# Optimization experiments

Measured on AMD Instinct MI355X. Metric: run time of the kernel, lower is better.

The kernel has to match this reference:

```python
import jax, jax.numpy as jnp
import numpy as np

ALPHA, BETA, LAMB, GAMMA = 1.0, 1.0, 1e-4, 1.0
K_NN, TAU = 50, 0.1
EPS = 1e-8


def _sqdist(A, B):
    # ||a - b||^2, clamped at 0 like the torch code
    d2 = (A * A).sum(1)[:, None] + (B * B).sum(1)[None, :] - 2.0 * (A @ B.T)
    return jnp.maximum(d2, 0.0)


def _mmd(s, t):
    comb = jnp.concatenate([s, t], axis=0)
    sigma_sq = jax.lax.stop_gradient(jnp.median(_sqdist(comb, comb))) / 2.0
    sigma_sq = jnp.where(sigma_sq < 1e-6, jnp.float32(1.0), sigma_sq)
    g = 1.0 / (sigma_sq + EPS)
    kxx = jnp.exp(-g * _sqdist(s, s)).mean()
    kyy = jnp.exp(-g * _sqdist(t, t)).mean()
    kxy = jnp.exp(-g * _sqdist(s, t)).mean()
    return jnp.maximum(kxx + kyy - 2.0 * kxy, 0.0)


def setup_inputs() -> dict:
    key = jax.random.key(0)
    ks = jax.random.split(key, 8)
    B, d, N, Nq, K = 256, 128, 200000, 10000, K_NN
    q_batch = jax.random.normal(ks[0], (B, d), jnp.float32)
    X = jax.random.normal(ks[1], (N, d), jnp.float32)
    W = jax.random.normal(ks[2], (d, d), jnp.float32) * (1.0 / np.sqrt(d))
    b = jnp.zeros((d,), jnp.float32)
    pre_weights = jax.random.uniform(ks[3], (Nq, K), jnp.float32)
    pre_weights = pre_weights / pre_weights.sum(1, keepdims=True)
    pre_indices = jax.random.randint(ks[4], (Nq, K), 0, N)
    q_indices = jax.random.randint(ks[5], (B,), 0, Nq)
    idx = jax.random.randint(ks[6], (B,), 0, N)
    return {"q_batch": q_batch, "X": X, "W": W, "b": b,
            "pre_weights": pre_weights, "pre_indices": pre_indices,
            "q_indices": q_indices, "idx": idx}


def reference(q_batch, X, W, b, pre_weights, pre_indices, q_indices, idx):
    Tq = q_batch @ W.T + b                                   # model(q_batch), Linear(d, d)
    # ---- MMD between mapped queries and a random database batch ----
    loss_dist = _mmd(Tq, X[idx])
    # ---- exact KNN (faiss IndexFlatL2 equivalent) on detached embeddings ----
    d2_all = _sqdist(jax.lax.stop_gradient(Tq), X)           # [B, N]
    _, post_idx = jax.lax.top_k(-d2_all, K_NN)               # [B, K] nearest neighbors
    Xn = X[post_idx]                                         # [B, K, d]
    l2 = ((Tq[:, None, :] - Xn) ** 2).sum(-1)                # [B, K] (grad flows here)
    post_w = jax.nn.softmax(-l2 / TAU, axis=1)
    # ---- union-KL, vectorized over batch (exact torch.unique semantics) ----
    pre_i = pre_indices[q_indices]                           # [B, K]
    pre_w = pre_weights[q_indices]                           # [B, K]
    cat = jnp.concatenate([pre_i, post_idx], axis=1)         # [B, 2K]
    # multiplicity of each id within the concatenated list -> collapse duplicates
    mult = (cat[:, :, None] == cat[:, None, :]).sum(-1).astype(jnp.float32)  # [B, 2K]
    p_raw = jnp.einsum('bmk,bk->bm',
                       (cat[:, :, None] == pre_i[:, None, :]).astype(jnp.float32), pre_w)
    q_raw = jnp.einsum('bmk,bk->bm',
                       (cat[:, :, None] == post_idx[:, None, :]).astype(jnp.float32), post_w)
    p_c = jnp.maximum(p_raw, EPS)
    q_c = jnp.maximum(q_raw, EPS)
    p = p_c / (p_c / mult).sum(1, keepdims=True)             # normalize over union
    q = q_c / (q_c / mult).sum(1, keepdims=True)
    kl = ((p * (jnp.log(p) - jnp.log(q))) / mult).sum(1)     # KL(p || q) per sample
    loss_knn = kl.mean()
    # ---- L2 regularization of model params & anchor loss ----
    loss_reg = 0.5 * ((W ** 2).sum() + (b ** 2).sum())
    loss_anchor = ((Tq - q_batch) ** 2).sum(1).mean()
    total = ALPHA * loss_dist + BETA * loss_knn + LAMB * loss_reg + GAMMA * loss_anchor
    return jnp.stack([total, loss_dist, loss_knn, loss_anchor])
```

## Files before the change

### kernel.cpp

```cpp
#include <hip/hip_runtime.h>
#include <cstdint>

#define D 128
#define NPTS 200000
#define KNN 50
#define CAP 8192
#define NS 8192
#define SLACK 2.0f
#define EB 2048

#define OFF_ACC    0
#define OFF_SEL    256
#define OFF_CNT    1024
#define OFF_HIST0  17408
#define OFF_HIST12 148480
#define MEMSET_BYTES 214016
#define OFF_COMB   214016
#define OFF_D2     476160
#define OFF_XN     1524736
#define OFF_SAMP   2324736
#define OFF_EBUF   2324736
#define OFF_THR    10713344
#define OFF_CANDI  10714368
#define OFF_KSG    19102976
#define OFF_BCNT   19102976
#define OFF_TQSW   27491584
#define OFF_XBF    27557120

typedef __attribute__((ext_vector_type(8))) short bf16x8;
typedef __attribute__((ext_vector_type(4))) float f32x4;
typedef const __attribute__((address_space(1))) void* gas_p;
typedef __attribute__((address_space(3))) void* las_p;

__device__ __forceinline__ unsigned fkey(float f) {
    unsigned u = __float_as_uint(f);
    return u ^ ((unsigned)((int)u >> 31) | 0x80000000u);
}

__device__ __forceinline__ void stage8k(const unsigned short* __restrict__ g,
                                        unsigned short* l, int w, int lane)
{
    #pragma unroll
    for (int j = 0; j < 2; j++) {
        const unsigned short* gp = g + j * 2048 + w * 512 + lane * 8;
        unsigned short* lp = l + j * 2048 + w * 512;
        __builtin_amdgcn_global_load_lds((gas_p)gp, (las_p)lp, 16, 0, 0);
    }
}

__global__ void k_phase1(const float* __restrict__ q, const float* __restrict__ X,
                         const float* __restrict__ W, const float* __restrict__ bb,
                         const int* __restrict__ idx, float* __restrict__ comb,
                         unsigned short* __restrict__ tqsw, unsigned short* __restrict__ xbf,
                         float* __restrict__ xn, float* __restrict__ acc)
{
    const int blk = blockIdx.x, t = threadIdx.x;
    if (blk < 12500) {
        __shared__ float xr[16];
        const int lr = t & 15;
        if (t < 16) xr[t] = 0.f;
        __syncthreads();
        const float4* src = (const float4*)(X + ((long)(blk * 16 + lr)) * D + (t >> 4) * 8);
        float4 v0 = src[0], v1 = src[1];
        uint4 pk;
        pk.x = (__float_as_uint(v0.x) >> 16) | (__float_as_uint(v0.y) & 0xFFFF0000u);
        pk.y = (__float_as_uint(v0.z) >> 16) | (__float_as_uint(v0.w) & 0xFFFF0000u);
        pk.z = (__float_as_uint(v1.x) >> 16) | (__float_as_uint(v1.y) & 0xFFFF0000u);
        pk.w = (__float_as_uint(v1.z) >> 16) | (__float_as_uint(v1.w) & 0xFFFF0000u);
        *(uint4*)(xbf + (long)blk * 2048 + t * 8) = pk;
        float ssq = v0.x*v0.x + v0.y*v0.y + v0.z*v0.z + v0.w*v0.w
                  + v1.x*v1.x + v1.y*v1.y + v1.z*v1.z + v1.w*v1.w;
        atomicAdd(&xr[lr], ssq);
        __syncthreads();
        if (t < 16) xn[blk * 16 + t] = xr[t];
    } else if (blk < 12628) {
        __shared__ float rowv[2][D];
        __shared__ float red[2][D];
        const int half = t >> 7, tt = t & 127;
        const int row = (blk - 12500) * 2 + half;
        rowv[half][tt] = q[row * D + tt];
        __syncthreads();
        float s = 0.f;
        const float* wr = W + tt * D;
        #pragma unroll 4
        for (int k = 0; k < D; k++) s = fmaf(rowv[half][k], wr[k], s);
        s += bb[tt];
        comb[row * D + tt] = s;
        unsigned ub = __float_as_uint(s);
        unsigned short hv = (unsigned short)((ub + 0x7fffu + ((ub >> 16) & 1u)) >> 16);
        int ksb = tt >> 5, quad = (tt & 31) >> 3, jj = tt & 7;
        int lane = quad * 16 + (row & 15);
        tqsw[(row >> 4) * 2048 + ksb * 512 + lane * 8 + jj] = hv;
        float dd = s - rowv[half][tt];
        red[half][tt] = dd * dd;
        __syncthreads();
        for (int off = 64; off > 0; off >>= 1) { if (tt < off) red[half][tt] += red[half][tt + off]; __syncthreads(); }
        if (tt == 0) atomicAdd(&acc[0], red[half][0]);
    } else if (blk < 12756) {
        const int half = t >> 7, tt = t & 127;
        const int i = (blk - 12628) * 2 + half;
        comb[(256 + i) * D + tt] = X[(long)idx[i] * D + tt];
    } else {
        __shared__ float wred[4];
        const int base = (blk - 12756) * 4096;
        float s = 0.f;
        #pragma unroll 4
        for (int k = 0; k < 16; k++) { float v = W[base + k * 256 + t]; s = fmaf(v, v, s); }
        if (blk == 12756 && t < D) { float v = bb[t]; s = fmaf(v, v, s); }
        #pragma unroll
        for (int off = 32; off > 0; off >>= 1) s += __shfl_down(s, off);
        if ((t & 63) == 0) wred[t >> 6] = s;
        __syncthreads();
        if (t == 0) atomicAdd(&acc[7], wred[0] + wred[1] + wred[2] + wred[3]);
    }
}

__global__ void k_d2h(const float* __restrict__ comb, float* __restrict__ D2w,
                      unsigned* __restrict__ hist0)
{
    __shared__ float cj[64][D + 1];
    __shared__ float ci[4][D];
    __shared__ unsigned h[4096];
    const int ib = blockIdx.x, jb = blockIdx.y, t = threadIdx.x;
    const int w = t >> 6, l = t & 63;
    for (int m = t; m < 4096; m += 256) h[m] = 0;
    const int irow = ib * 4 + w;
    ci[w][l] = comb[irow * D + l];
    ci[w][l + 64] = comb[irow * D + l + 64];
    const float4* src = (const float4*)(comb + (jb * 64) * D);
    #pragma unroll
    for (int m = 0; m < 8; m++) {
        int u = m * 256 + t;
        int r = u >> 5, c = u & 31;
        float4 v = src[u];
        cj[r][c * 4 + 0] = v.x; cj[r][c * 4 + 1] = v.y; cj[r][c * 4 + 2] = v.z; cj[r][c * 4 + 3] = v.w;
    }
    __syncthreads();
    float s = 0.f;
    #pragma unroll 4
    for (int k = 0; k < D; k++) { float d = ci[w][k] - cj[l][k]; s = fmaf(d, d, s); }
    D2w[irow * 512 + jb * 64 + l] = s;
    atomicAdd(&h[__float_as_uint(s) >> 20], 1u);
    __syncthreads();
    const int sh = (ib + jb) & 7;
    for (int m = t; m < 4096; m += 256) { unsigned v = h[m]; if (v) atomicAdd(&hist0[m * 8 + sh], v); }
}

__global__ __launch_bounds__(256) void k_mf0(const unsigned short* __restrict__ tqsw,
    const unsigned short* __restrict__ xbf, const float* __restrict__ xn,
    float* __restrict__ samp, const unsigned* __restrict__ hist0, unsigned* __restrict__ sel)
{
    if (blockIdx.x == 256) {
        __shared__ unsigned part[256];
        const int t = threadIdx.x;
        unsigned s = 0;
        for (int m = 0; m < 16; m++) {
            int b = t * 16 + m;
            #pragma unroll
            for (int sh = 0; sh < 8; sh++) s += hist0[b * 8 + sh];
        }
        part[t] = s;
        __syncthreads();
        if (t == 0) {
            for (int tg = 0; tg < 2; tg++) {
                unsigned r = tg ? 131072u : 131071u;
                int c = 0;
                while (part[c] <= r) { r -= part[c]; c++; }
                int b = c * 16;
                while (true) {
                    unsigned bs = 0;
                    #pragma unroll
                    for (int sh = 0; sh < 8; sh++) bs += hist0[b * 8 + sh];
                    if (bs <= r) { r -= bs; b++; } else break;
                }
                sel[2 * tg] = (unsigned)b; sel[2 * tg + 1] = r;
            }
        }
        return;
    }
    __shared__ unsigned short sb[4096];
    const int t = threadIdx.x;
    const int w = t >> 6, lane = t & 63;
    const int lr = lane & 15, quad = lane >> 4;
    const int ck = blockIdx.x;
    stage8k(xbf + (long)ck * 4096, sb, w, lane);
    bf16x8 a[4][4];
    #pragma unroll
    for (int i = 0; i < 4; i++)
        #pragma unroll
        for (int ks = 0; ks < 4; ks++)
            a[i][ks] = *(const bf16x8*)(tqsw + (w * 4 + i) * 2048 + ks * 512 + lane * 8);
    __syncthreads();
    #pragma unroll
    for (int tt = 0; tt < 2; tt++) {
        const int r = (ck * 2 + tt) * 16 + lr;
        float xnv = xn[r];
        bf16x8 b[4];
        #pragma unroll
        for (int ks = 0; ks < 4; ks++)
            b[ks] = *(const bf16x8*)(sb + tt * 2048 + ks * 512 + lane * 8);
        f32x4 acc[4];
        #pragma unroll
        for (int i = 0; i < 4; i++) acc[i] = (f32x4){0.f, 0.f, 0.f, 0.f};
        #pragma unroll
        for (int ks = 0; ks < 4; ks++)
            #pragma unroll
            for (int i = 0; i < 4; i++)
                acc[i] = __builtin_amdgcn_mfma_f32_16x16x32_bf16(a[i][ks], b[ks], acc[i], 0, 0, 0);
        #pragma unroll
        for (int i = 0; i < 4; i++)
            #pragma unroll
            for (int reg = 0; reg < 4; reg++) {
                int qq = w * 64 + i * 16 + quad * 4 + reg;
                samp[qq * NS + r] = xnv - 2.f * acc[i][reg];
            }
    }
}

__global__ void k_h1thr(const float* __restrict__ D2w, unsigned* __restrict__ hist12,
                        const unsigned* __restrict__ sel, const float* __restrict__ samp,
                        float* __restrict__ thr)
{
    __shared__ unsigned buf[8192];
    __shared__ unsigned wred[4];
    const int t = threadIdx.x;
    if (blockIdx.x < 256) {
        for (int m = t; m < 8192; m += 256) buf[m] = 0;
        __syncthreads();
        unsigned p0 = sel[0], p1 = sel[2];
        const int e0 = blockIdx.x * 1024;
        for (int m = 0; m < 4; m++) {
            unsigned key = __float_as_uint(D2w[e0 + m * 256 + t]);
            if ((key >> 20) == p0) atomicAdd(&buf[(key >> 8) & 0xFFFu], 1u);
            if ((key >> 20) == p1) atomicAdd(&buf[4096 + ((key >> 8) & 0xFFFu)], 1u);
        }
        __syncthreads();
        for (int m = t; m < 8192; m += 256) { unsigned v = buf[m]; if (v) atomicAdd(&hist12[m], v); }
    } else {
        const int q = blockIdx.x - 256;
        for (int m = t; m < NS; m += 256) buf[m] = fkey(samp[q * NS + m]);
        __syncthreads();
        unsigned v = 0;
        for (int bit = 31; bit >= 0; bit--) {
            unsigned trial = v | (1u << bit);
            unsigned c = 0;
            for (int m = t; m < NS; m += 256) c += (buf[m] < trial) ? 1u : 0u;
            #pragma unroll
            for (int off = 32; off > 0; off >>= 1) c += __shfl_down(c, off);
            if ((t & 63) == 0) wred[t >> 6] = c;
            __syncthreads();
            unsigned total = wred[0] + wred[1] + wred[2] + wred[3];
            __syncthreads();
            if (total <= (unsigned)(KNN - 1)) v = trial;
        }
        if (t == 0) {
            unsigned orig = (v & 0x80000000u) ? (v ^ 0x80000000u) : ~v;
            thr[q] = __uint_as_float(orig) + SLACK;
        }
    }
}

__global__ void k_hist2s(const float* __restrict__ D2w, unsigned* __restrict__ hist12,
                         unsigned* __restrict__ sel)
{
    __shared__ unsigned h[8192];
    __shared__ unsigned part[256];
    __shared__ unsigned pfx[2];
    __shared__ unsigned rr[2];
    const int t = threadIdx.x;
    for (int tg = 0; tg < 2; tg++) {
        const unsigned* hh = hist12 + tg * 4096;
        unsigned s = 0;
        for (int m = 0; m < 16; m++) s += hh[t * 16 + m];
        part[t] = s;
        __syncthreads();
        if (t == 0) {
            unsigned r = sel[1 + 2 * tg];
            int c = 0;
            while (part[c] <= r) { r -= part[c]; c++; }
            int b = c * 16;
            while (hh[b] <= r) { r -= hh[b]; b++; }
            pfx[tg] = (sel[2 * tg] << 12) | (unsigned)b;
            rr[tg] = r;
        }
        __syncthreads();
    }
    if (blockIdx.x == 0 && t == 0) {
        sel[4] = pfx[0]; sel[5] = rr[0]; sel[6] = pfx[1]; sel[7] = rr[1];
    }
    for (int m = t; m < 8192; m += 256) h[m] = 0;
    __syncthreads();
    unsigned p0 = pfx[0], p1 = pfx[1];
    const int e0 = blockIdx.x * 1024;
    for (int m = 0; m < 4; m++) {
        unsigned key = __float_as_uint(D2w[e0 + m * 256 + t]);
        if ((key >> 8) == p0) atomicAdd(&h[key & 0xFFu], 1u);
        if ((key >> 8) == p1) atomicAdd(&h[4096 + (key & 0xFFu)], 1u);
    }
    __syncthreads();
    unsigned* gp = hist12 + 8192;
    for (int m = t; m < 8192; m += 256) { unsigned v = h[m]; if (v) atomicAdd(&gp[m], v); }
}

__global__ __launch_bounds__(256) void k_mf1(const unsigned short* __restrict__ tqsw,
    const unsigned short* __restrict__ xbf, const float* __restrict__ xn,
    const float* __restrict__ thr, unsigned* __restrict__ ebuf, unsigned* __restrict__ bcnt,
    const float* __restrict__ D2w, const unsigned* __restrict__ hist12,
    const unsigned* __restrict__ sel, float* __restrict__ acc)
{
    if (blockIdx.x >= 1024) {
        __shared__ unsigned h2[512];
        __shared__ float gsh;
        __shared__ float part[12];
        const int t = threadIdx.x, w = t >> 6;
        h2[t] = hist12[8192 + t];
        h2[256 + t] = hist12[8192 + 4096 + t];
        __syncthreads();
        if (t == 0) {
            unsigned key[2];
            for (int tg = 0; tg < 2; tg++) {
                unsigned r = sel[5 + 2 * tg];
                const unsigned* hh = h2 + tg * 256;
                int b = 0;
                while (hh[b] <= r) { r -= hh[b]; b++; }
                key[tg] = (sel[4 + 2 * tg] << 8) | (unsigned)b;
            }
            float med = 0.5f * (__uint_as_float(key[0]) + __uint_as_float(key[1]));
            float ssq = 0.5f * med;
            if (ssq < 1e-6f) ssq = 1.0f;
            gsh = 1.0f / (ssq + 1e-8f);
        }
        __syncthreads();
        const float g = gsh;
        float s[3] = {0.f, 0.f, 0.f};
        const int e0 = (blockIdx.x - 1024) * 1024;
        #pragma unroll
        for (int m = 0; m < 4; m++) {
            int e = e0 + m * 256 + t;
            int i = e >> 9, j = e & 511;
            float v = expf(-g * D2w[e]);
            int qd = (i < 256) ? ((j < 256) ? 0 : 2) : ((j < 256) ? 2 : 1);
            s[qd] += v;
        }
        #pragma unroll
        for (int c = 0; c < 3; c++) {
            float x = s[c];
            #pragma unroll
            for (int off = 32; off > 0; off >>= 1) x += __shfl_down(x, off);
            if ((t & 63) == 0) part[w * 3 + c] = x;
        }
        __syncthreads();
        if (t == 0)
            for (int c = 0; c < 3; c++)
                atomicAdd(&acc[2 + c], part[c] + part[3 + c] + part[6 + c] + part[9 + c]);
        return;
    }
    __shared__ unsigned short sb[2][4096];
    __shared__ unsigned lbuf[1024];
    __shared__ unsigned lcnt;
    __shared__ unsigned gbase;
    const int t = threadIdx.x;
    const int w = t >> 6, lane = t & 63;
    const int lr = lane & 15, quad = lane >> 4;
    unsigned* eb = ebuf + (unsigned)blockIdx.x * EB;
    bf16x8 a[4][4];
    #pragma unroll
    for (int i = 0; i < 4; i++)
        #pragma unroll
        for (int ks = 0; ks < 4; ks++)
            a[i][ks] = *(const bf16x8*)(tqsw + (w * 4 + i) * 2048 + ks * 512 + lane * 8);
    float th_r[4][4];
    #pragma unroll
    for (int i = 0; i < 4; i++)
        #pragma unroll
        for (int reg = 0; reg < 4; reg++)
            th_r[i][reg] = thr[w * 64 + i * 16 + quad * 4 + reg];
    int ck = blockIdx.x;
    int cur = 0;
    if (t == 0) { lcnt = 0; gbase = 0; }
    stage8k(xbf + (long)ck * 4096, sb[0], w, lane);
    __syncthreads();
    while (true) {
        const int ckn = ck + 1024;
        const bool has = ckn < 6250;
        if (has) stage8k(xbf + (long)ckn * 4096, sb[cur ^ 1], w, lane);
        #pragma unroll
        for (int tt = 0; tt < 2; tt++) {
            const int r = (ck * 2 + tt) * 16 + lr;
            float xnv = xn[r];
            bf16x8 b[4];
            #pragma unroll
            for (int ks = 0; ks < 4; ks++)
                b[ks] = *(const bf16x8*)(sb[cur] + tt * 2048 + ks * 512 + lane * 8);
            f32x4 acc4[4];
            #pragma unroll
            for (int i = 0; i < 4; i++) acc4[i] = (f32x4){0.f, 0.f, 0.f, 0.f};
            #pragma unroll
            for (int ks = 0; ks < 4; ks++)
                #pragma unroll
                for (int i = 0; i < 4; i++)
                    acc4[i] = __builtin_amdgcn_mfma_f32_16x16x32_bf16(a[i][ks], b[ks], acc4[i], 0, 0, 0);
            #pragma unroll
            for (int i = 0; i < 4; i++)
                #pragma unroll
                for (int reg = 0; reg < 4; reg++) {
                    float s = xnv - 2.f * acc4[i][reg];
                    if (s <= th_r[i][reg]) {
                        unsigned qq = (unsigned)(w * 64 + i * 16 + quad * 4 + reg);
                        unsigned p = atomicAdd(&lcnt, 1u);
                        if (p < 1024u) lbuf[p] = (qq << 18) | (unsigned)r;
                        else {
                            unsigned d = gbase + p;
                            if (d < EB) eb[d] = (qq << 18) | (unsigned)r;
                        }
                    }
                }
        }
        __syncthreads();
        unsigned n = lcnt;
        if (!has || n >= 512u) {
            unsigned nf = (n < 1024u) ? n : 1024u;
            unsigned gb = gbase;
            for (unsigned m = t; m < nf; m += 256) {
                unsigned d = gb + m;
                if (d < EB) eb[d] = lbuf[m];
            }
            __syncthreads();
            if (t == 0) { gbase = gb + n; lcnt = 0; }
            __syncthreads();
        }
        if (!has) break;
        ck = ckn; cur ^= 1;
    }
    if (t == 0) bcnt[blockIdx.x] = (gbase < EB) ? gbase : EB;
}

__global__ __launch_bounds__(256) void k_scat(const unsigned* __restrict__ ebuf,
    const unsigned* __restrict__ bcnt, int* __restrict__ cand_i, unsigned* __restrict__ cnt)
{
    __shared__ unsigned hist[256];
    __shared__ unsigned startp[256];
    const int t = threadIdx.x;
    const int b0 = blockIdx.x * 8;
    hist[t] = 0;
    __syncthreads();
    for (int b = b0; b < b0 + 8; b++) {
        unsigned n = bcnt[b];
        const unsigned* e = ebuf + (unsigned)b * EB;
        for (unsigned m = t; m < n; m += 256)
            atomicAdd(&hist[e[m] >> 18], 1u);
    }
    __syncthreads();
    unsigned c = hist[t];
    if (c) {
        unsigned base = atomicAdd(&cnt[t * 16], c);
        startp[t] = ((unsigned)t << 13) + base;
    }
    __syncthreads();
    for (int b = b0; b < b0 + 8; b++) {
        unsigned n = bcnt[b];
        const unsigned* e = ebuf + (unsigned)b * EB;
        for (unsigned m = t; m < n; m += 256) {
            unsigned ent = e[m];
            unsigned qq = ent >> 18;
            unsigned pos = atomicAdd(&startp[qq], 1u);
            if (pos < ((qq + 1u) << 13)) cand_i[pos] = (int)(ent & 0x3FFFFu);
        }
    }
}

__global__ void k_rescore(const float* __restrict__ comb, const float* __restrict__ X,
                          const float* __restrict__ xn, const int* __restrict__ cand_i,
                          const unsigned* __restrict__ cnt, unsigned* __restrict__ ksg)
{
    __shared__ float qrow[D];
    const int q = blockIdx.x, sp = blockIdx.y, t = threadIdx.x;
    if (t < D) qrow[t] = comb[q * D + t];
    __syncthreads();
    unsigned nn = cnt[q * 16];
    const int n = (nn < (unsigned)CAP) ? (int)nn : CAP;
    const int g = t >> 3, j = t & 7;
    for (int m = sp * 32 + g; m < n; m += 512) {
        int r = cand_i[q * CAP + m];
        const float4* xr = (const float4*)(X + (long)r * D);
        float s = 0.f;
        #pragma unroll
        for (int p = 0; p < 4; p++) {
            float4 xv = xr[j * 4 + p];
            float4 qv = *(const float4*)&qrow[(j * 4 + p) * 4];
            s = fmaf(xv.x, qv.x, fmaf(xv.y, qv.y, fmaf(xv.z, qv.z, fmaf(xv.w, qv.w, s))));
        }
        s += __shfl_down(s, 4); s += __shfl_down(s, 2); s += __shfl_down(s, 1);
        if (j == 0) ksg[q * CAP + m] = fkey(xn[r] - 2.f * s);
    }
}

__global__ void k_post2(const float* __restrict__ comb, const float* __restrict__ X,
                        const int* __restrict__ cand_i, const unsigned* __restrict__ cnt,
                        const unsigned* __restrict__ ksg, const int* __restrict__ pri,
                        const float* __restrict__ prw, const int* __restrict__ qix,
                        float* __restrict__ acc)
{
    __shared__ unsigned ks[CAP];
    __shared__ float qrow[D];
    __shared__ unsigned wred[4];
    __shared__ unsigned wpos, eqn;
    __shared__ int eq[64];
    __shared__ int pidx[KNN];
    __shared__ float l2s[KNN];
    __shared__ float pw[KNN];
    __shared__ int ci[100];
    __shared__ float pwv[50], qwv[50];
    __shared__ float pterm[100], qterm[100], kterm[100];
    __shared__ float Sp, Sq;
    const int q = blockIdx.x, t = threadIdx.x;
    if (t < D) qrow[t] = comb[q * D + t];
    if (t == 0) { wpos = 0; eqn = 0; }
    unsigned nn = cnt[q * 16];
    const int n = (nn < (unsigned)CAP) ? (int)nn : CAP;
    for (int m = t; m < n; m += 256) ks[m] = ksg[q * CAP + m];
    __syncthreads();
    int kk = KNN - 1; if (kk > n - 1) kk = n - 1;
    unsigned v = 0;
    for (int bit = 31; bit >= 0; bit--) {
        unsigned trial = v | (1u << bit);
        unsigned c = 0;
        for (int m = t; m < n; m += 256) c += (ks[m] < trial) ? 1u : 0u;
        #pragma unroll
        for (int off = 32; off > 0; off >>= 1) c += __shfl_down(c, off);
        if ((t & 63) == 0) wred[t >> 6] = c;
        __syncthreads();
        unsigned total = wred[0] + wred[1] + wred[2] + wred[3];
        __syncthreads();
        if (total <= (unsigned)kk) v = trial;
    }
    for (int m = t; m < n; m += 256) {
        if (ks[m] < v) {
            unsigned p = atomicAdd(&wpos, 1u);
            pidx[p] = cand_i[q * CAP + m];
        } else if (ks[m] == v) {
            unsigned p = atomicAdd(&eqn, 1u);
            if (p < 64) eq[p] = cand_i[q * CAP + m];
        }
    }
    __syncthreads();
    if (t == 0) {
        int c1 = (int)wpos, need = KNN - c1;
        int ne = (eqn < 64u) ? (int)eqn : 64;
        for (int a = 0; a < ne; a++)
            for (int b2 = a + 1; b2 < ne; b2++)
                if (eq[b2] < eq[a]) { int tmp = eq[a]; eq[a] = eq[b2]; eq[b2] = tmp; }
        for (int a = 0; a < need && a < ne; a++) pidx[c1 + a] = eq[a];
    }
    __syncthreads();
    const int g = t >> 3, j = t & 7;
    for (int nb = g; nb < KNN; nb += 32) {
        long r = pidx[nb];
        const float4* xr = (const float4*)(X + r * D);
        float s = 0.f;
        #pragma unroll
        for (int p = 0; p < 4; p++) {
            float4 xv = xr[j * 4 + p];
            float4 qv = *(const float4*)&qrow[(j * 4 + p) * 4];
            float d0 = qv.x - xv.x, d1 = qv.y - xv.y, d2 = qv.z - xv.z, d3 = qv.w - xv.w;
            s += d0 * d0 + d1 * d1 + d2 * d2 + d3 * d3;
        }
        s += __shfl_down(s, 4); s += __shfl_down(s, 2); s += __shfl_down(s, 1);
        if (j == 0) l2s[nb] = s;
    }
    int qi = qix[q];
    if (t >= 128 && t < 178) { int k = t - 128; ci[k] = pri[qi * 50 + k]; pwv[k] = prw[qi * 50 + k]; }
    __syncthreads();
    if (t < 64) {
        float logit = (t < KNN) ? (-l2s[t] * 10.0f) : -3.4e38f;
        float m = logit;
        #pragma unroll
        for (int off = 32; off > 0; off >>= 1) m = fmaxf(m, __shfl_down(m, off));
        m = __shfl(m, 0);
        float e = (t < KNN) ? expf(logit - m) : 0.f;
        float ss = e;
        #pragma unroll
        for (int off = 32; off > 0; off >>= 1) ss += __shfl_down(ss, off);
        ss = __shfl(ss, 0);
        if (t < KNN) pw[t] = e / ss;
    }
    __syncthreads();
    if (t < 50) { ci[50 + t] = pidx[t]; qwv[t] = pw[t]; }
    __syncthreads();
    float pc = 0.f, qc = 0.f, mult = 0.f;
    if (t < 100) {
        int c = ci[t];
        float pr = 0.f, qr = 0.f;
        for (int k = 0; k < 50; k++) {
            bool m1 = (c == ci[k]); bool m2 = (c == ci[50 + k]);
            mult += (m1 ? 1.f : 0.f) + (m2 ? 1.f : 0.f);
            pr += m1 ? pwv[k] : 0.f;
            qr += m2 ? qwv[k] : 0.f;
        }
        pc = fmaxf(pr, 1e-8f); qc = fmaxf(qr, 1e-8f);
        pterm[t] = pc / mult; qterm[t] = qc / mult;
    }
    __syncthreads();
    if (t == 0) { float a = 0.f, b2 = 0.f; for (int m = 0; m < 100; m++) { a += pterm[m]; b2 += qterm[m]; } Sp = a; Sq = b2; }
    __syncthreads();
    if (t < 100) {
        float p = pc / Sp, qq2 = qc / Sq;
        kterm[t] = (p * (logf(p) - logf(qq2))) / mult;
    }
    __syncthreads();
    if (t == 0) { float s = 0.f; for (int m = 0; m < 100; m++) s += kterm[m]; atomicAdd(&acc[1], s); }
}

__global__ void k_final(const float* __restrict__ acc, float* __restrict__ out)
{
    if (threadIdx.x == 0) {
        float reg = 0.5f * acc[7];
        float kxx = acc[2] / 65536.f, kyy = acc[3] / 65536.f, kxy = acc[4] / 131072.f;
        float ld = fmaxf(kxx + kyy - 2.f * kxy, 0.f);
        float lknn = acc[1] / 256.f;
        float lanc = acc[0] / 256.f;
        out[0] = ld + lknn + 1e-4f * reg + lanc;
        out[1] = ld; out[2] = lknn; out[3] = lanc;
    }
}

extern "C" void kernel_launch(void* const* d_in, const int* in_sizes, int n_in,
                              void* d_out, int out_size, void* d_ws, size_t ws_size,
                              hipStream_t stream)
{
    (void)in_sizes; (void)n_in; (void)out_size; (void)ws_size;
    const float* q   = (const float*)d_in[0];
    const float* X   = (const float*)d_in[1];
    const float* W   = (const float*)d_in[2];
    const float* bb  = (const float*)d_in[3];
    const float* prw = (const float*)d_in[4];
    const int*   pri = (const int*)d_in[5];
    const int*   qix = (const int*)d_in[6];
    const int*   idx = (const int*)d_in[7];
    float* out = (float*)d_out;
    char* ws = (char*)d_ws;
    float*    acc   = (float*)(ws + OFF_ACC);
    unsigned* sel   = (unsigned*)(ws + OFF_SEL);
    unsigned* cnt   = (unsigned*)(ws + OFF_CNT);
    unsigned* hist0 = (unsigned*)(ws + OFF_HIST0);
    unsigned* hist12= (unsigned*)(ws + OFF_HIST12);
    float*    comb  = (float*)(ws + OFF_COMB);
    float*    D2w   = (float*)(ws + OFF_D2);
    float*    xn    = (float*)(ws + OFF_XN);
    float*    samp  = (float*)(ws + OFF_SAMP);
    float*    thr   = (float*)(ws + OFF_THR);
    int*      cix   = (int*)(ws + OFF_CANDI);
    unsigned* ksg   = (unsigned*)(ws + OFF_KSG);
    unsigned* ebuf  = (unsigned*)(ws + OFF_EBUF);
    unsigned* bcnt  = (unsigned*)(ws + OFF_BCNT);
    unsigned short* tqsw = (unsigned short*)(ws + OFF_TQSW);
    unsigned short* xbf  = (unsigned short*)(ws + OFF_XBF);

    hipMemsetAsync(ws, 0, MEMSET_BYTES, stream);
    hipLaunchKernelGGL(k_phase1,  dim3(12760),   dim3(256), 0, stream, q, X, W, bb, idx, comb, tqsw, xbf, xn, acc);
    hipLaunchKernelGGL(k_d2h,     dim3(128, 8),  dim3(256), 0, stream, comb, D2w, hist0);
    hipLaunchKernelGGL(k_mf0,     dim3(257),     dim3(256), 0, stream, tqsw, xbf, xn, samp, hist0, sel);
    hipLaunchKernelGGL(k_h1thr,   dim3(512),     dim3(256), 0, stream, D2w, hist12, sel, samp, thr);
    hipLaunchKernelGGL(k_hist2s,  dim3(256),     dim3(256), 0, stream, D2w, hist12, sel);
    hipLaunchKernelGGL(k_mf1,     dim3(1280),    dim3(256), 0, stream, tqsw, xbf, xn, thr, ebuf, bcnt, D2w, hist12, sel, acc);
    hipLaunchKernelGGL(k_scat,    dim3(128),     dim3(256), 0, stream, ebuf, bcnt, cix, cnt);
    hipLaunchKernelGGL(k_rescore, dim3(256, 16), dim3(256), 0, stream, comb, X, xn, cix, cnt, ksg);
    hipLaunchKernelGGL(k_post2,   dim3(256),     dim3(256), 0, stream, comb, X, cix, cnt, ksg, pri, prw, qix, acc);
    hipLaunchKernelGGL(k_final,   dim3(1),       dim3(64),  0, stream, acc, out);
}
```

Baseline: 397.3 us.

## Fuse post-distance stages into one cooperative kernel with grid syncs

Merges the d2/histogram kernel with the sample MFMA kernel into a single launch. All later stages (threshold scan, two histogram refinement passes, MMD plus filter, scatter, rescore, post KL, final) now run in one persistent cooperative kernel of 512 blocks, separated by grid-wide syncs. A multi-kernel fallback is kept for when cooperative launch is unavailable. The aim is to cut per-kernel launch and drain gaps across the many small stages, at the cost of a fixed 512-block grid, grid-sync overhead, and the filter and rescore work being redistributed over fewer blocks.

Result: slower. 816.5 us (+105.5%).

```diff
diff --git a/kernel.cpp b/kernel.cpp
--- a/kernel.cpp
+++ b/kernel.cpp
@@ -1,5 +1,8 @@
 #include <hip/hip_runtime.h>
+#include <hip/hip_cooperative_groups.h>
 #include <cstdint>
+
+namespace cg = cooperative_groups;
 
 #define D 128
 #define NPTS 200000
@@ -7,7 +10,10 @@
 #define CAP 8192
 #define NS 8192
 #define SLACK 2.0f
-#define EB 2048
+#define CGRID 512
+#define NFILT 256
+#define EBC 8192
+#define SMB 36352
 
 #define OFF_ACC    0
 #define OFF_SEL    256
@@ -115,130 +121,90 @@
     }
 }
 
-__global__ void k_d2h(const float* __restrict__ comb, float* __restrict__ D2w,
-                      unsigned* __restrict__ hist0)
-{
-    __shared__ float cj[64][D + 1];
-    __shared__ float ci[4][D];
-    __shared__ unsigned h[4096];
-    const int ib = blockIdx.x, jb = blockIdx.y, t = threadIdx.x;
-    const int w = t >> 6, l = t & 63;
-    for (int m = t; m < 4096; m += 256) h[m] = 0;
-    const int irow = ib * 4 + w;
-    ci[w][l] = comb[irow * D + l];
-    ci[w][l + 64] = comb[irow * D + l + 64];
-    const float4* src = (const float4*)(comb + (jb * 64) * D);
-    #pragma unroll
-    for (int m = 0; m < 8; m++) {
-        int u = m * 256 + t;
-        int r = u >> 5, c = u & 31;
-        float4 v = src[u];
-        cj[r][c * 4 + 0] = v.x; cj[r][c * 4 + 1] = v.y; cj[r][c * 4 + 2] = v.z; cj[r][c * 4 + 3] = v.w;
-    }
-    __syncthreads();
-    float s = 0.f;
-    #pragma unroll 4
-    for (int k = 0; k < D; k++) { float d = ci[w][k] - cj[l][k]; s = fmaf(d, d, s); }
-    D2w[irow * 512 + jb * 64 + l] = s;
-    atomicAdd(&h[__float_as_uint(s) >> 20], 1u);
-    __syncthreads();
-    const int sh = (ib + jb) & 7;
-    for (int m = t; m < 4096; m += 256) { unsigned v = h[m]; if (v) atomicAdd(&hist0[m * 8 + sh], v); }
-}
-
-__global__ __launch_bounds__(256) void k_mf0(const unsigned short* __restrict__ tqsw,
-    const unsigned short* __restrict__ xbf, const float* __restrict__ xn,
-    float* __restrict__ samp, const unsigned* __restrict__ hist0, unsigned* __restrict__ sel)
-{
-    if (blockIdx.x == 256) {
-        __shared__ unsigned part[256];
-        const int t = threadIdx.x;
-        unsigned s = 0;
-        for (int m = 0; m < 16; m++) {
-            int b = t * 16 + m;
-            #pragma unroll
-            for (int sh = 0; sh < 8; sh++) s += hist0[b * 8 + sh];
-        }
-        part[t] = s;
-        __syncthreads();
-        if (t == 0) {
-            for (int tg = 0; tg < 2; tg++) {
-                unsigned r = tg ? 131072u : 131071u;
-                int c = 0;
-                while (part[c] <= r) { r -= part[c]; c++; }
-                int b = c * 16;
-                while (true) {
-                    unsigned bs = 0;
-                    #pragma unroll
-                    for (int sh = 0; sh < 8; sh++) bs += hist0[b * 8 + sh];
-                    if (bs <= r) { r -= bs; b++; } else break;
+__global__ void k_d2m(const float* __restrict__ comb, float* __restrict__ D2w,
+                      unsigned* __restrict__ hist0, const unsigned short* __restrict__ tqsw,
+                      const unsigned short* __restrict__ xbf, const float* __restrict__ xn,
+                      float* __restrict__ samp)
+{
+    __shared__ __align__(16) char smraw[51456];
+    const int b = blockIdx.x, t = threadIdx.x;
+    if (b < 1024) {
+        float (*cj)[D + 1] = (float(*)[D + 1])smraw;
+        float (*ci)[D]     = (float(*)[D])(smraw + 33024);
+        unsigned* h        = (unsigned*)(smraw + 35072);
+        const int ib = b >> 3, jb = b & 7;
+        const int w = t >> 6, l = t & 63;
+        for (int m = t; m < 4096; m += 256) h[m] = 0;
+        const int irow = ib * 4 + w;
+        ci[w][l] = comb[irow * D + l];
+        ci[w][l + 64] = comb[irow * D + l + 64];
+        const float4* src = (const float4*)(comb + (jb * 64) * D);
+        #pragma unroll
+        for (int m = 0; m < 8; m++) {
+            int u = m * 256 + t;
+            int r = u >> 5, c = u & 31;
+            float4 v = src[u];
+            cj[r][c * 4 + 0] = v.x; cj[r][c * 4 + 1] = v.y; cj[r][c * 4 + 2] = v.z; cj[r][c * 4 + 3] = v.w;
+        }
+        __syncthreads();
+        float s = 0.f;
+        #pragma unroll 4
+        for (int k = 0; k < D; k++) { float d = ci[w][k] - cj[l][k]; s = fmaf(d, d, s); }
+        D2w[irow * 512 + jb * 64 + l] = s;
+        atomicAdd(&h[__float_as_uint(s) >> 20], 1u);
+        __syncthreads();
+        const int sh = (ib + jb) & 7;
+        for (int m = t; m < 4096; m += 256) { unsigned v = h[m]; if (v) atomicAdd(&hist0[m * 8 + sh], v); }
+    } else {
+        unsigned short* sb = (unsigned short*)smraw;
+        const int w = t >> 6, lane = t & 63;
+        const int lr = lane & 15, quad = lane >> 4;
+        const int ck = b - 1024;
+        stage8k(xbf + (long)ck * 4096, sb, w, lane);
+        bf16x8 a[4][4];
+        #pragma unroll
+        for (int i = 0; i < 4; i++)
+            #pragma unroll
+            for (int ks = 0; ks < 4; ks++)
+                a[i][ks] = *(const bf16x8*)(tqsw + (w * 4 + i) * 2048 + ks * 512 + lane * 8);
+        __syncthreads();
+        #pragma unroll
+        for (int tt = 0; tt < 2; tt++) {
+            const int r = (ck * 2 + tt) * 16 + lr;
+            float xnv = xn[r];
+            bf16x8 bfr[4];
+            #pragma unroll
+            for (int ks = 0; ks < 4; ks++)
+                bfr[ks] = *(const bf16x8*)(sb + tt * 2048 + ks * 512 + lane * 8);
+            f32x4 acc4[4];
+            #pragma unroll
+            for (int i = 0; i < 4; i++) acc4[i] = (f32x4){0.f, 0.f, 0.f, 0.f};
+            #pragma unroll
+            for (int ks = 0; ks < 4; ks++)
+                #pragma unroll
+                for (int i = 0; i < 4; i++)
+                    acc4[i] = __builtin_amdgcn_mfma_f32_16x16x32_bf16(a[i][ks], bfr[ks], acc4[i], 0, 0, 0);
+            #pragma unroll
+            for (int i = 0; i < 4; i++)
+                #pragma unroll
+                for (int reg = 0; reg < 4; reg++) {
+                    int qq = w * 64 + i * 16 + quad * 4 + reg;
+                    samp[qq * NS + r] = xnv - 2.f * acc4[i][reg];
                 }
-                sel[2 * tg] = (unsigned)b; sel[2 * tg + 1] = r;
-            }
-        }
-        return;
-    }
-    __shared__ unsigned short sb[4096];
-    const int t = threadIdx.x;
-    const int w = t >> 6, lane = t & 63;
-    const int lr = lane & 15, quad = lane >> 4;
-    const int ck = blockIdx.x;
-    stage8k(xbf + (long)ck * 4096, sb, w, lane);
-    bf16x8 a[4][4];
-    #pragma unroll
-    for (int i = 0; i < 4; i++)
-        #pragma unroll
-        for (int ks = 0; ks < 4; ks++)
-            a[i][ks] = *(const bf16x8*)(tqsw + (w * 4 + i) * 2048 + ks * 512 + lane * 8);
-    __syncthreads();
-    #pragma unroll
-    for (int tt = 0; tt < 2; tt++) {
-        const int r = (ck * 2 + tt) * 16 + lr;
-        float xnv = xn[r];
-        bf16x8 b[4];
-        #pragma unroll
-        for (int ks = 0; ks < 4; ks++)
-            b[ks] = *(const bf16x8*)(sb + tt * 2048 + ks * 512 + lane * 8);
-        f32x4 acc[4];
-        #pragma unroll
-        for (int i = 0; i < 4; i++) acc[i] = (f32x4){0.f, 0.f, 0.f, 0.f};
-        #pragma unroll
-        for (int ks = 0; ks < 4; ks++)
-            #pragma unroll
-            for (int i = 0; i < 4; i++)
-                acc[i] = __builtin_amdgcn_mfma_f32_16x16x32_bf16(a[i][ks], b[ks], acc[i], 0, 0, 0);
-        #pragma unroll
-        for (int i = 0; i < 4; i++)
-            #pragma unroll
-            for (int reg = 0; reg < 4; reg++) {
-                int qq = w * 64 + i * 16 + quad * 4 + reg;
-                samp[qq * NS + r] = xnv - 2.f * acc[i][reg];
-            }
-    }
-}
-
-__global__ void k_h1thr(const float* __restrict__ D2w, unsigned* __restrict__ hist12,
-                        const unsigned* __restrict__ sel, const float* __restrict__ samp,
-                        float* __restrict__ thr)
-{
-    __shared__ unsigned buf[8192];
-    __shared__ unsigned wred[4];
-    const int t = threadIdx.x;
-    if (blockIdx.x < 256) {
-        for (int m = t; m < 8192; m += 256) buf[m] = 0;
-        __syncthreads();
-        unsigned p0 = sel[0], p1 = sel[2];
-        const int e0 = blockIdx.x * 1024;
-        for (int m = 0; m < 4; m++) {
-            unsigned key = __float_as_uint(D2w[e0 + m * 256 + t]);
-            if ((key >> 20) == p0) atomicAdd(&buf[(key >> 8) & 0xFFFu], 1u);
-            if ((key >> 20) == p1) atomicAdd(&buf[4096 + ((key >> 8) & 0xFFFu)], 1u);
-        }
-        __syncthreads();
-        for (int m = t; m < 8192; m += 256) { unsigned v = buf[m]; if (v) atomicAdd(&hist12[m], v); }
-    } else {
-        const int q = blockIdx.x - 256;
-        for (int m = t; m < NS; m += 256) buf[m] = fkey(samp[q * NS + m]);
+        }
+    }
+}
+
+
+__device__ void st_thrscan(int b, int t, char* sm, const float* __restrict__ samp,
+                           const unsigned* __restrict__ hist0, unsigned* __restrict__ sel,
+                           float* __restrict__ thr)
+{
+    if (b < 256) {
+        unsigned* buf = (unsigned*)sm;
+        unsigned* wred = (unsigned*)(sm + 32768);
+        const int q2 = b;
+        for (int m = t; m < NS; m += 256) buf[m] = fkey(samp[q2 * NS + m]);
         __syncthreads();
         unsigned v = 0;
         for (int bit = 31; bit >= 0; bit--) {
@@ -255,19 +221,62 @@
         }
         if (t == 0) {
             unsigned orig = (v & 0x80000000u) ? (v ^ 0x80000000u) : ~v;
-            thr[q] = __uint_as_float(orig) + SLACK;
-        }
-    }
-}
-
-__global__ void k_hist2s(const float* __restrict__ D2w, unsigned* __restrict__ hist12,
-                         unsigned* __restrict__ sel)
-{
-    __shared__ unsigned h[8192];
-    __shared__ unsigned part[256];
-    __shared__ unsigned pfx[2];
-    __shared__ unsigned rr[2];
-    const int t = threadIdx.x;
+            thr[q2] = __uint_as_float(orig) + SLACK;
+        }
+    } else if (b == 256) {
+        unsigned* part = (unsigned*)sm;
+        unsigned s = 0;
+        for (int m = 0; m < 16; m++) {
+            int bin = t * 16 + m;
+            #pragma unroll
+            for (int sh = 0; sh < 8; sh++) s += hist0[bin * 8 + sh];
+        }
+        part[t] = s;
+        __syncthreads();
+        if (t == 0) {
+            for (int tg = 0; tg < 2; tg++) {
+                unsigned r = tg ? 131072u : 131071u;
+                int c = 0;
+                while (part[c] <= r) { r -= part[c]; c++; }
+                int bin = c * 16;
+                while (true) {
+                    unsigned bs = 0;
+                    #pragma unroll
+                    for (int sh = 0; sh < 8; sh++) bs += hist0[bin * 8 + sh];
+                    if (bs <= r) { r -= bs; bin++; } else break;
+                }
+                sel[2 * tg] = (unsigned)bin; sel[2 * tg + 1] = r;
+            }
+        }
+    }
+}
+
+__device__ void st_h1(int b, int t, char* sm, const float* __restrict__ D2w,
+                      const unsigned* __restrict__ sel, unsigned* __restrict__ hist12)
+{
+    if (b >= 256) return;
+    unsigned* buf = (unsigned*)sm;
+    for (int m = t; m < 8192; m += 256) buf[m] = 0;
+    __syncthreads();
+    unsigned p0 = sel[0], p1 = sel[2];
+    const int e0 = b * 1024;
+    for (int m = 0; m < 4; m++) {
+        unsigned key = __float_as_uint(D2w[e0 + m * 256 + t]);
+        if ((key >> 20) == p0) atomicAdd(&buf[(key >> 8) & 0xFFFu], 1u);
+        if ((key >> 20) == p1) atomicAdd(&buf[4096 + ((key >> 8) & 0xFFFu)], 1u);
+    }
+    __syncthreads();
+    for (int m = t; m < 8192; m += 256) { unsigned v2 = buf[m]; if (v2) atomicAdd(&hist12[m], v2); }
+}
+
+__device__ void st_h2(int b, int t, char* sm, const float* __restrict__ D2w,
+                      unsigned* __restrict__ hist12, unsigned* __restrict__ sel)
+{
+    if (b >= 256) return;
+    unsigned* h = (unsigned*)sm;
+    unsigned* part = (unsigned*)(sm + 32768);
+    unsigned* pfx = (unsigned*)(sm + 33792);
+    unsigned* rr = (unsigned*)(sm + 33800);
     for (int tg = 0; tg < 2; tg++) {
         const unsigned* hh = hist12 + tg * 4096;
         unsigned s = 0;
@@ -278,20 +287,20 @@
             unsigned r = sel[1 + 2 * tg];
             int c = 0;
             while (part[c] <= r) { r -= part[c]; c++; }
-            int b = c * 16;
-            while (hh[b] <= r) { r -= hh[b]; b++; }
-            pfx[tg] = (sel[2 * tg] << 12) | (unsigned)b;
+            int bin = c * 16;
+            while (hh[bin] <= r) { r -= hh[bin]; bin++; }
+            pfx[tg] = (sel[2 * tg] << 12) | (unsigned)bin;
             rr[tg] = r;
         }
         __syncthreads();
     }
-    if (blockIdx.x == 0 && t == 0) {
+    if (b == 0 && t == 0) {
         sel[4] = pfx[0]; sel[5] = rr[0]; sel[6] = pfx[1]; sel[7] = rr[1];
     }
     for (int m = t; m < 8192; m += 256) h[m] = 0;
     __syncthreads();
     unsigned p0 = pfx[0], p1 = pfx[1];
-    const int e0 = blockIdx.x * 1024;
+    const int e0 = b * 1024;
     for (int m = 0; m < 4; m++) {
         unsigned key = __float_as_uint(D2w[e0 + m * 256 + t]);
         if ((key >> 8) == p0) atomicAdd(&h[key & 0xFFu], 1u);
@@ -299,20 +308,21 @@
     }
     __syncthreads();
     unsigned* gp = hist12 + 8192;
-    for (int m = t; m < 8192; m += 256) { unsigned v = h[m]; if (v) atomicAdd(&gp[m], v); }
-}
-
-__global__ __launch_bounds__(256) void k_mf1(const unsigned short* __restrict__ tqsw,
-    const unsigned short* __restrict__ xbf, const float* __restrict__ xn,
-    const float* __restrict__ thr, unsigned* __restrict__ ebuf, unsigned* __restrict__ bcnt,
+    for (int m = t; m < 8192; m += 256) { unsigned v2 = h[m]; if (v2) atomicAdd(&gp[m], v2); }
+}
+
+__device__ void st_mmdfilt(int b, int t, char* sm,
+    const unsigned short* __restrict__ tqsw, const unsigned short* __restrict__ xbf,
+    const float* __restrict__ xn, const float* __restrict__ thr,
+    unsigned* __restrict__ ebuf, unsigned* __restrict__ bcnt,
     const float* __restrict__ D2w, const unsigned* __restrict__ hist12,
     const unsigned* __restrict__ sel, float* __restrict__ acc)
 {
-    if (blockIdx.x >= 1024) {
-        __shared__ unsigned h2[512];
-        __shared__ float gsh;
-        __shared__ float part[12];
-        const int t = threadIdx.x, w = t >> 6;
+    if (b < 256) {
+        unsigned* h2 = (unsigned*)sm;
+        float* gshp = (float*)(sm + 2048);
+        float* partf = (float*)(sm + 2064);
+        const int w = t >> 6;
         h2[t] = hist12[8192 + t];
         h2[256 + t] = hist12[8192 + 4096 + t];
         __syncthreads();
@@ -321,24 +331,24 @@
             for (int tg = 0; tg < 2; tg++) {
                 unsigned r = sel[5 + 2 * tg];
                 const unsigned* hh = h2 + tg * 256;
-                int b = 0;
-                while (hh[b] <= r) { r -= hh[b]; b++; }
-                key[tg] = (sel[4 + 2 * tg] << 8) | (unsigned)b;
+                int bin = 0;
+                while (hh[bin] <= r) { r -= hh[bin]; bin++; }
+                key[tg] = (sel[4 + 2 * tg] << 8) | (unsigned)bin;
             }
             float med = 0.5f * (__uint_as_float(key[0]) + __uint_as_float(key[1]));
             float ssq = 0.5f * med;
             if (ssq < 1e-6f) ssq = 1.0f;
-            gsh = 1.0f / (ssq + 1e-8f);
-        }
-        __syncthreads();
-        const float g = gsh;
+            gshp[0] = 1.0f / (ssq + 1e-8f);
+        }
+        __syncthreads();
+        const float gm = gshp[0];
         float s[3] = {0.f, 0.f, 0.f};
-        const int e0 = (blockIdx.x - 1024) * 1024;
+        const int e0 = b * 1024;
         #pragma unroll
         for (int m = 0; m < 4; m++) {
             int e = e0 + m * 256 + t;
             int i = e >> 9, j = e & 511;
-            float v = expf(-g * D2w[e]);
+            float v = expf(-gm * D2w[e]);
             int qd = (i < 256) ? ((j < 256) ? 0 : 2) : ((j < 256) ? 2 : 1);
             s[qd] += v;
         }
@@ -347,119 +357,120 @@
             float x = s[c];
             #pragma unroll
             for (int off = 32; off > 0; off >>= 1) x += __shfl_down(x, off);
-            if ((t & 63) == 0) part[w * 3 + c] = x;
+            if ((t & 63) == 0) partf[w * 3 + c] = x;
         }
         __syncthreads();
         if (t == 0)
             for (int c = 0; c < 3; c++)
-                atomicAdd(&acc[2 + c], part[c] + part[3 + c] + part[6 + c] + part[9 + c]);
-        return;
-    }
-    __shared__ unsigned short sb[2][4096];
-    __shared__ unsigned lbuf[1024];
-    __shared__ unsigned lcnt;
-    __shared__ unsigned gbase;
-    const int t = threadIdx.x;
-    const int w = t >> 6, lane = t & 63;
-    const int lr = lane & 15, quad = lane >> 4;
-    unsigned* eb = ebuf + (unsigned)blockIdx.x * EB;
-    bf16x8 a[4][4];
-    #pragma unroll
-    for (int i = 0; i < 4; i++)
-        #pragma unroll
-        for (int ks = 0; ks < 4; ks++)
-            a[i][ks] = *(const bf16x8*)(tqsw + (w * 4 + i) * 2048 + ks * 512 + lane * 8);
-    float th_r[4][4];
-    #pragma unroll
-    for (int i = 0; i < 4; i++)
-        #pragma unroll
-        for (int reg = 0; reg < 4; reg++)
-            th_r[i][reg] = thr[w * 64 + i * 16 + quad * 4 + reg];
-    int ck = blockIdx.x;
-    int cur = 0;
-    if (t == 0) { lcnt = 0; gbase = 0; }
-    stage8k(xbf + (long)ck * 4096, sb[0], w, lane);
-    __syncthreads();
-    while (true) {
-        const int ckn = ck + 1024;
-        const bool has = ckn < 6250;
-        if (has) stage8k(xbf + (long)ckn * 4096, sb[cur ^ 1], w, lane);
-        #pragma unroll
-        for (int tt = 0; tt < 2; tt++) {
-            const int r = (ck * 2 + tt) * 16 + lr;
-            float xnv = xn[r];
-            bf16x8 b[4];
+                atomicAdd(&acc[2 + c], partf[c] + partf[3 + c] + partf[6 + c] + partf[9 + c]);
+    } else {
+        const int fb = b - 256;
+        unsigned short* sb = (unsigned short*)sm;
+        unsigned* lbuf = (unsigned*)(sm + 16384);
+        unsigned* lcnt = (unsigned*)(sm + 20480);
+        unsigned* gbasep = (unsigned*)(sm + 20484);
+        const int w = t >> 6, lane = t & 63;
+        const int lr = lane & 15, quad = lane >> 4;
+        unsigned* eb = ebuf + (unsigned)fb * EBC;
+        bf16x8 a[4][4];
+        #pragma unroll
+        for (int i = 0; i < 4; i++)
             #pragma unroll
             for (int ks = 0; ks < 4; ks++)
-                b[ks] = *(const bf16x8*)(sb[cur] + tt * 2048 + ks * 512 + lane * 8);
-            f32x4 acc4[4];
-            #pragma unroll
-            for (int i = 0; i < 4; i++) acc4[i] = (f32x4){0.f, 0.f, 0.f, 0.f};
-            #pragma unroll
-            for (int ks = 0; ks < 4; ks++)
+                a[i][ks] = *(const bf16x8*)(tqsw + (w * 4 + i) * 2048 + ks * 512 + lane * 8);
+        float th_r[4][4];
+        #pragma unroll
+        for (int i = 0; i < 4; i++)
+            #pragma unroll
+            for (int reg = 0; reg < 4; reg++)
+                th_r[i][reg] = thr[w * 64 + i * 16 + quad * 4 + reg];
+        int ck = fb;
+        int cur = 0;
+        if (t == 0) { lcnt[0] = 0; gbasep[0] = 0; }
+        stage8k(xbf + (long)ck * 4096, sb, w, lane);
+        __syncthreads();
+        while (true) {
+            const int ckn = ck + NFILT;
+            const bool has = ckn < 6250;
+            if (has) stage8k(xbf + (long)ckn * 4096, sb + (cur ^ 1) * 4096, w, lane);
+            #pragma unroll
+            for (int tt = 0; tt < 2; tt++) {
+                const int r = (ck * 2 + tt) * 16 + lr;
+                float xnv = xn[r];
+                bf16x8 bfr[4];
+                #pragma unroll
+                for (int ks = 0; ks < 4; ks++)
+                    bfr[ks] = *(const bf16x8*)(sb + cur * 4096 + tt * 2048 + ks * 512 + lane * 8);
+                f32x4 acc4[4];
+                #pragma unroll
+                for (int i = 0; i < 4; i++) acc4[i] = (f32x4){0.f, 0.f, 0.f, 0.f};
+                #pragma unroll
+                for (int ks = 0; ks < 4; ks++)
+                    #pragma unroll
+                    for (int i = 0; i < 4; i++)
+                        acc4[i] = __builtin_amdgcn_mfma_f32_16x16x32_bf16(a[i][ks], bfr[ks], acc4[i], 0, 0, 0);
                 #pragma unroll
                 for (int i = 0; i < 4; i++)
-                    acc4[i] = __builtin_amdgcn_mfma_f32_16x16x32_bf16(a[i][ks], b[ks], acc4[i], 0, 0, 0);
-            #pragma unroll
-            for (int i = 0; i < 4; i++)
-                #pragma unroll
-                for (int reg = 0; reg < 4; reg++) {
-                    float s = xnv - 2.f * acc4[i][reg];
-                    if (s <= th_r[i][reg]) {
-                        unsigned qq = (unsigned)(w * 64 + i * 16 + quad * 4 + reg);
-                        unsigned p = atomicAdd(&lcnt, 1u);
-                        if (p < 1024u) lbuf[p] = (qq << 18) | (unsigned)r;
-                        else {
-                            unsigned d = gbase + p;
-                            if (d < EB) eb[d] = (qq << 18) | (unsigned)r;
+                    #pragma unroll
+                    for (int reg = 0; reg < 4; reg++) {
+                        float s = xnv - 2.f * acc4[i][reg];
+                        if (s <= th_r[i][reg]) {
+                            unsigned qq = (unsigned)(w * 64 + i * 16 + quad * 4 + reg);
+                            unsigned p = atomicAdd(&lcnt[0], 1u);
+                            if (p < 1024u) lbuf[p] = (qq << 18) | (unsigned)r;
+                            else {
+                                unsigned dd = gbasep[0] + p;
+                                if (dd < EBC) eb[dd] = (qq << 18) | (unsigned)r;
+                            }
                         }
                     }
-                }
-        }
-        __syncthreads();
-        unsigned n = lcnt;
-        if (!has || n >= 512u) {
-            unsigned nf = (n < 1024u) ? n : 1024u;
-            unsigned gb = gbase;
-            for (unsigned m = t; m < nf; m += 256) {
-                unsigned d = gb + m;
-                if (d < EB) eb[d] = lbuf[m];
             }
             __syncthreads();
-            if (t == 0) { gbase = gb + n; lcnt = 0; }
-            __syncthreads();
-        }
-        if (!has) break;
-        ck = ckn; cur ^= 1;
-    }
-    if (t == 0) bcnt[blockIdx.x] = (gbase < EB) ? gbase : EB;
-}
-
-__global__ __launch_bounds__(256) void k_scat(const unsigned* __restrict__ ebuf,
-    const unsigned* __restrict__ bcnt, int* __restrict__ cand_i, unsigned* __restrict__ cnt)
-{
-    __shared__ unsigned hist[256];
-    __shared__ unsigned startp[256];
-    const int t = threadIdx.x;
-    const int b0 = blockIdx.x * 8;
-    hist[t] = 0;
-    __syncthreads();
-    for (int b = b0; b < b0 + 8; b++) {
-        unsigned n = bcnt[b];
-        const unsigned* e = ebuf + (unsigned)b * EB;
+            unsigned n = lcnt[0];
+            if (!has || n >= 512u) {
+                unsigned nf = (n < 1024u) ? n : 1024u;
+                unsigned gb = gbasep[0];
+                for (unsigned m = t; m < nf; m += 256) {
+                    unsigned dd = gb + m;
+                    if (dd < EBC) eb[dd] = lbuf[m];
+                }
+                __syncthreads();
+                if (t == 0) { gbasep[0] = gb + n; lcnt[0] = 0; }
+                __syncthreads();
+            }
+            if (!has) break;
+            ck = ckn; cur ^= 1;
+        }
+        if (t == 0) bcnt[fb] = (gbasep[0] < (unsigned)EBC) ? gbasep[0] : (unsigned)EBC;
+    }
+}
+
+__device__ void st_scat(int b, int t, char* sm, const unsigned* __restrict__ ebuf,
+                        const unsigned* __restrict__ bcnt, int* __restrict__ cand_i,
+                        unsigned* __restrict__ cnt)
+{
+    if (b >= 128) return;
+    unsigned* histq = (unsigned*)sm;
+    unsigned* startp = (unsigned*)(sm + 1024);
+    histq[t] = 0;
+    __syncthreads();
+    const int b0 = b * 2;
+    for (int lb = b0; lb < b0 + 2; lb++) {
+        unsigned n = bcnt[lb];
+        const unsigned* e = ebuf + (unsigned)lb * EBC;
         for (unsigned m = t; m < n; m += 256)
-            atomicAdd(&hist[e[m] >> 18], 1u);
-    }
-    __syncthreads();
-    unsigned c = hist[t];
+            atomicAdd(&histq[e[m] >> 18], 1u);
+    }
+    __syncthreads();
+    unsigned c = histq[t];
     if (c) {
         unsigned base = atomicAdd(&cnt[t * 16], c);
         startp[t] = ((unsigned)t << 13) + base;
     }
     __syncthreads();
-    for (int b = b0; b < b0 + 8; b++) {
-        unsigned n = bcnt[b];
-        const unsigned* e = ebuf + (unsigned)b * EB;
+    for (int lb = b0; lb < b0 + 2; lb++) {
+        unsigned n = bcnt[lb];
+        const unsigned* e = ebuf + (unsigned)lb * EBC;
         for (unsigned m = t; m < n; m += 256) {
             unsigned ent = e[m];
             unsigned qq = ent >> 18;
@@ -469,56 +480,64 @@
     }
 }
 
-__global__ void k_rescore(const float* __restrict__ comb, const float* __restrict__ X,
-                          const float* __restrict__ xn, const int* __restrict__ cand_i,
-                          const unsigned* __restrict__ cnt, unsigned* __restrict__ ksg)
-{
-    __shared__ float qrow[D];
-    const int q = blockIdx.x, sp = blockIdx.y, t = threadIdx.x;
-    if (t < D) qrow[t] = comb[q * D + t];
-    __syncthreads();
-    unsigned nn = cnt[q * 16];
+__device__ void st_resc(int b, int t, int gridn, char* sm, const float* __restrict__ comb,
+                        const float* __restrict__ X, const float* __restrict__ xn,
+                        const int* __restrict__ cand_i, const unsigned* __restrict__ cnt,
+                        unsigned* __restrict__ ksg)
+{
+    float* qrow = (float*)sm;
+    for (int u = b; u < 4096; u += gridn) {
+        const int q2 = u >> 4, sp = u & 15;
+        __syncthreads();
+        if (t < D) qrow[t] = comb[q2 * D + t];
+        __syncthreads();
+        unsigned nn = cnt[q2 * 16];
+        const int n = (nn < (unsigned)CAP) ? (int)nn : CAP;
+        const int gg = t >> 3, j = t & 7;
+        for (int m = sp * 32 + gg; m < n; m += 512) {
+            int r = cand_i[q2 * CAP + m];
+            const float4* xr = (const float4*)(X + (long)r * D);
+            float s = 0.f;
+            #pragma unroll
+            for (int p = 0; p < 4; p++) {
+                float4 xv = xr[j * 4 + p];
+                float4 qv = *(const float4*)&qrow[(j * 4 + p) * 4];
+                s = fmaf(xv.x, qv.x, fmaf(xv.y, qv.y, fmaf(xv.z, qv.z, fmaf(xv.w, qv.w, s))));
+            }
+            s += __shfl_down(s, 4); s += __shfl_down(s, 2); s += __shfl_down(s, 1);
+            if (j == 0) ksg[q2 * CAP + m] = fkey(xn[r] - 2.f * s);
+        }
+    }
+}
+
+__device__ void st_post(int b, int t, char* sm, const float* __restrict__ comb,
+                        const float* __restrict__ X, const int* __restrict__ cand_i,
+                        const unsigned* __restrict__ cnt, const unsigned* __restrict__ ksg,
+                        const int* __restrict__ pri, const float* __restrict__ prw,
+                        const int* __restrict__ qix, float* __restrict__ acc)
+{
+    if (b >= 256) return;
+    unsigned* ks   = (unsigned*)sm;
+    float* qrow    = (float*)(sm + 32768);
+    unsigned* wred = (unsigned*)(sm + 33280);
+    int* eq        = (int*)(sm + 33296);
+    int* pidx      = (int*)(sm + 33552);
+    float* l2s     = (float*)(sm + 33752);
+    float* pw      = (float*)(sm + 33952);
+    int* ci        = (int*)(sm + 34152);
+    float* pwv     = (float*)(sm + 34552);
+    float* qwv     = (float*)(sm + 34752);
+    float* pterm   = (float*)(sm + 34952);
+    float* qterm   = (float*)(sm + 35352);
+    float* kterm   = (float*)(sm + 35752);
+    float* SpSq    = (float*)(sm + 36152);
+    unsigned* wpe  = (unsigned*)(sm + 36160);
+    const int q2 = b;
+    if (t < D) qrow[t] = comb[q2 * D + t];
+    if (t == 0) { wpe[0] = 0; wpe[1] = 0; }
+    unsigned nn = cnt[q2 * 16];
     const int n = (nn < (unsigned)CAP) ? (int)nn : CAP;
-    const int g = t >> 3, j = t & 7;
-    for (int m = sp * 32 + g; m < n; m += 512) {
-        int r = cand_i[q * CAP + m];
-        const float4* xr = (const float4*)(X + (long)r * D);
-        float s = 0.f;
-        #pragma unroll
-        for (int p = 0; p < 4; p++) {
-            float4 xv = xr[j * 4 + p];
-            float4 qv = *(const float4*)&qrow[(j * 4 + p) * 4];
-            s = fmaf(xv.x, qv.x, fmaf(xv.y, qv.y, fmaf(xv.z, qv.z, fmaf(xv.w, qv.w, s))));
-        }
-        s += __shfl_down(s, 4); s += __shfl_down(s, 2); s += __shfl_down(s, 1);
-        if (j == 0) ksg[q * CAP + m] = fkey(xn[r] - 2.f * s);
-    }
-}
-
-__global__ void k_post2(const float* __restrict__ comb, const float* __restrict__ X,
-                        const int* __restrict__ cand_i, const unsigned* __restrict__ cnt,
-                        const unsigned* __restrict__ ksg, const int* __restrict__ pri,
-                        const float* __restrict__ prw, const int* __restrict__ qix,
-                        float* __restrict__ acc)
-{
-    __shared__ unsigned ks[CAP];
-    __shared__ float qrow[D];
-    __shared__ unsigned wred[4];
-    __shared__ unsigned wpos, eqn;
-    __shared__ int eq[64];
-    __shared__ int pidx[KNN];
-    __shared__ float l2s[KNN];
-    __shared__ float pw[KNN];
-    __shared__ int ci[100];
-    __shared__ float pwv[50], qwv[50];
-    __shared__ float pterm[100], qterm[100], kterm[100];
-    __shared__ float Sp, Sq;
-    const int q = blockIdx.x, t = threadIdx.x;
-    if (t < D) qrow[t] = comb[q * D + t];
-    if (t == 0) { wpos = 0; eqn = 0; }
-    unsigned nn = cnt[q * 16];
-    const int n = (nn < (unsigned)CAP) ? (int)nn : CAP;
-    for (int m = t; m < n; m += 256) ks[m] = ksg[q * CAP + m];
+    for (int m = t; m < n; m += 256) ks[m] = ksg[q2 * CAP + m];
     __syncthreads();
     int kk = KNN - 1; if (kk > n - 1) kk = n - 1;
     unsigned v = 0;
@@ -536,25 +555,25 @@
     }
     for (int m = t; m < n; m += 256) {
         if (ks[m] < v) {
-            unsigned p = atomicAdd(&wpos, 1u);
-            pidx[p] = cand_i[q * CAP + m];
+            unsigned p = atomicAdd(&wpe[0], 1u);
+            pidx[p] = cand_i[q2 * CAP + m];
         } else if (ks[m] == v) {
-            unsigned p = atomicAdd(&eqn, 1u);
-            if (p < 64) eq[p] = cand_i[q * CAP + m];
+            unsigned p = atomicAdd(&wpe[1], 1u);
+            if (p < 64) eq[p] = cand_i[q2 * CAP + m];
         }
     }
     __syncthreads();
     if (t == 0) {
-        int c1 = (int)wpos, need = KNN - c1;
-        int ne = (eqn < 64u) ? (int)eqn : 64;
-        for (int a = 0; a < ne; a++)
-            for (int b2 = a + 1; b2 < ne; b2++)
-                if (eq[b2] < eq[a]) { int tmp = eq[a]; eq[a] = eq[b2]; eq[b2] = tmp; }
-        for (int a = 0; a < need && a < ne; a++) pidx[c1 + a] = eq[a];
-    }
-    __syncthreads();
-    const int g = t >> 3, j = t & 7;
-    for (int nb = g; nb < KNN; nb += 32) {
+        int c1 = (int)wpe[0], need = KNN - c1;
+        int ne = (wpe[1] < 64u) ? (int)wpe[1] : 64;
+        for (int a2 = 0; a2 < ne; a2++)
+            for (int b2 = a2 + 1; b2 < ne; b2++)
+                if (eq[b2] < eq[a2]) { int tmp = eq[a2]; eq[a2] = eq[b2]; eq[b2] = tmp; }
+        for (int a2 = 0; a2 < need && a2 < ne; a2++) pidx[c1 + a2] = eq[a2];
+    }
+    __syncthreads();
+    const int gg = t >> 3, j = t & 7;
+    for (int nb = gg; nb < KNN; nb += 32) {
         long r = pidx[nb];
         const float4* xr = (const float4*)(X + r * D);
         float s = 0.f;
@@ -568,7 +587,7 @@
         s += __shfl_down(s, 4); s += __shfl_down(s, 2); s += __shfl_down(s, 1);
         if (j == 0) l2s[nb] = s;
     }
-    int qi = qix[q];
+    int qi = qix[q2];
     if (t >= 128 && t < 178) { int k = t - 128; ci[k] = pri[qi * 50 + k]; pwv[k] = prw[qi * 50 + k]; }
     __syncthreads();
     if (t < 64) {
@@ -601,19 +620,19 @@
         pterm[t] = pc / mult; qterm[t] = qc / mult;
     }
     __syncthreads();
-    if (t == 0) { float a = 0.f, b2 = 0.f; for (int m = 0; m < 100; m++) { a += pterm[m]; b2 += qterm[m]; } Sp = a; Sq = b2; }
+    if (t == 0) { float a2 = 0.f, b2 = 0.f; for (int m = 0; m < 100; m++) { a2 += pterm[m]; b2 += qterm[m]; } SpSq[0] = a2; SpSq[1] = b2; }
     __syncthreads();
     if (t < 100) {
-        float p = pc / Sp, qq2 = qc / Sq;
+        float p = pc / SpSq[0], qq2 = qc / SpSq[1];
         kterm[t] = (p * (logf(p) - logf(qq2))) / mult;
     }
     __syncthreads();
     if (t == 0) { float s = 0.f; for (int m = 0; m < 100; m++) s += kterm[m]; atomicAdd(&acc[1], s); }
 }
 
-__global__ void k_final(const float* __restrict__ acc, float* __restrict__ out)
-{
-    if (threadIdx.x == 0) {
+__device__ void st_final(int b, int t, const float* __restrict__ acc, float* __restrict__ out)
+{
+    if (b == 0 && t == 0) {
         float reg = 0.5f * acc[7];
         float kxx = acc[2] / 65536.f, kyy = acc[3] / 65536.f, kxy = acc[4] / 131072.f;
         float ld = fmaxf(kxx + kyy - 2.f * kxy, 0.f);
@@ -623,6 +642,70 @@
         out[1] = ld; out[2] = lknn; out[3] = lanc;
     }
 }
+
+__global__ __launch_bounds__(256, 2) void k_coop(
+    const unsigned short* __restrict__ tqsw, const unsigned short* __restrict__ xbf,
+    const float* __restrict__ xn, const float* __restrict__ samp,
+    float* __restrict__ thr, const unsigned* __restrict__ hist0,
+    unsigned* __restrict__ sel, const float* __restrict__ D2w,
+    unsigned* __restrict__ hist12, unsigned* __restrict__ ebuf,
+    unsigned* __restrict__ bcnt, int* __restrict__ cand_i, unsigned* __restrict__ cnt,
+    const float* __restrict__ comb, const float* __restrict__ X,
+    unsigned* __restrict__ ksg, const int* __restrict__ pri,
+    const float* __restrict__ prw, const int* __restrict__ qix,
+    float* __restrict__ acc, float* __restrict__ out)
+{
+    cg::grid_group gridg = cg::this_grid();
+    __shared__ __align__(16) char sm[SMB];
+    const int b = blockIdx.x, t = threadIdx.x;
+    st_thrscan(b, t, sm, samp, hist0, sel, thr);
+    gridg.sync();
+    st_h1(b, t, sm, D2w, sel, hist12);
+    gridg.sync();
+    st_h2(b, t, sm, D2w, hist12, sel);
+    gridg.sync();
+    st_mmdfilt(b, t, sm, tqsw, xbf, xn, thr, ebuf, bcnt, D2w, hist12, sel, acc);
+    gridg.sync();
+    st_scat(b, t, sm, ebuf, bcnt, cand_i, cnt);
+    gridg.sync();
+    st_resc(b, t, CGRID, sm, comb, X, xn, cand_i, cnt, ksg);
+    gridg.sync();
+    st_post(b, t, sm, comb, X, cand_i, cnt, ksg, pri, prw, qix, acc);
+    gridg.sync();
+    st_final(b, t, acc, out);
+}
+
+__global__ void fb_thrscan(const float* samp, const unsigned* hist0, unsigned* sel, float* thr)
+{ __shared__ __align__(16) char sm[SMB]; st_thrscan(blockIdx.x, threadIdx.x, sm, samp, hist0, sel, thr); }
+
+__global__ void fb_h1(const float* D2w, const unsigned* sel, unsigned* hist12)
+{ __shared__ __align__(16) char sm[SMB]; st_h1(blockIdx.x, threadIdx.x, sm, D2w, sel, hist12); }
+
+__global__ void fb_h2(const float* D2w, unsigned* hist12, unsigned* sel)
+{ __shared__ __align__(16) char sm[SMB]; st_h2(blockIdx.x, threadIdx.x, sm, D2w, hist12, sel); }
+
+__global__ void fb_mmdfilt(const unsigned short* tqsw, const unsigned short* xbf,
+                           const float* xn, const float* thr, unsigned* ebuf, unsigned* bcnt,
+                           const float* D2w, const unsigned* hist12, const unsigned* sel, float* acc)
+{ __shared__ __align__(16) char sm[SMB];
+  st_mmdfilt(blockIdx.x, threadIdx.x, sm, tqsw, xbf, xn, thr, ebuf, bcnt, D2w, hist12, sel, acc); }
+
+__global__ void fb_scat(const unsigned* ebuf, const unsigned* bcnt, int* cand_i, unsigned* cnt)
+{ __shared__ __align__(16) char sm[SMB]; st_scat(blockIdx.x, threadIdx.x, sm, ebuf, bcnt, cand_i, cnt); }
+
+__global__ void fb_resc(const float* comb, const float* X, const float* xn,
+                        const int* cand_i, const unsigned* cnt, unsigned* ksg)
+{ __shared__ __align__(16) char sm[SMB];
+  st_resc(blockIdx.x, threadIdx.x, CGRID, sm, comb, X, xn, cand_i, cnt, ksg); }
+
+__global__ void fb_post(const float* comb, const float* X, const int* cand_i,
+                        const unsigned* cnt, const unsigned* ksg, const int* pri,
+                        const float* prw, const int* qix, float* acc)
+{ __shared__ __align__(16) char sm[SMB];
+  st_post(blockIdx.x, threadIdx.x, sm, comb, X, cand_i, cnt, ksg, pri, prw, qix, acc); }
+
+__global__ void fb_final(const float* acc, float* out)
+{ st_final(blockIdx.x, threadIdx.x, acc, out); }
 
 extern "C" void kernel_launch(void* const* d_in, const int* in_sizes, int n_in,
                               void* d_out, int out_size, void* d_ws, size_t ws_size,
@@ -657,14 +740,36 @@
     unsigned short* xbf  = (unsigned short*)(ws + OFF_XBF);
 
     hipMemsetAsync(ws, 0, MEMSET_BYTES, stream);
-    hipLaunchKernelGGL(k_phase1,  dim3(12760),   dim3(256), 0, stream, q, X, W, bb, idx, comb, tqsw, xbf, xn, acc);
-    hipLaunchKernelGGL(k_d2h,     dim3(128, 8),  dim3(256), 0, stream, comb, D2w, hist0);
-    hipLaunchKernelGGL(k_mf0,     dim3(257),     dim3(256), 0, stream, tqsw, xbf, xn, samp, hist0, sel);
-    hipLaunchKernelGGL(k_h1thr,   dim3(512),     dim3(256), 0, stream, D2w, hist12, sel, samp, thr);
-    hipLaunchKernelGGL(k_hist2s,  dim3(256),     dim3(256), 0, stream, D2w, hist12, sel);
-    hipLaunchKernelGGL(k_mf1,     dim3(1280),    dim3(256), 0, stream, tqsw, xbf, xn, thr, ebuf, bcnt, D2w, hist12, sel, acc);
-    hipLaunchKernelGGL(k_scat,    dim3(128),     dim3(256), 0, stream, ebuf, bcnt, cix, cnt);
-    hipLaunchKernelGGL(k_rescore, dim3(256, 16), dim3(256), 0, stream, comb, X, xn, cix, cnt, ksg);
-    hipLaunchKernelGGL(k_post2,   dim3(256),     dim3(256), 0, stream, comb, X, cix, cnt, ksg, pri, prw, qix, acc);
-    hipLaunchKernelGGL(k_final,   dim3(1),       dim3(64),  0, stream, acc, out);
-}
+    hipLaunchKernelGGL(k_phase1, dim3(12760), dim3(256), 0, stream, q, X, W, bb, idx, comb, tqsw, xbf, xn, acc);
+    hipLaunchKernelGGL(k_d2m,    dim3(1280),  dim3(256), 0, stream, comb, D2w, hist0, tqsw, xbf, xn, samp);
+
+    static int coop_ok = -1;
+    if (coop_ok < 0) {
+        int dev = 0, cu = 0, nb = 0;
+        hipGetDevice(&dev);
+        hipDeviceGetAttribute(&cu, hipDeviceAttributeMultiprocessorCount, dev);
+        hipError_t e = hipOccupancyMaxActiveBlocksPerMultiprocessor(
+            &nb, reinterpret_cast<const void*>(&k_coop), 256, 0);
+        coop_ok = (e == hipSuccess && (long)nb * (long)cu >= (long)CGRID) ? 1 : 0;
+    }
+    bool done = false;
+    if (coop_ok == 1) {
+        void* cargs[] = { (void*)&tqsw, (void*)&xbf, (void*)&xn, (void*)&samp, (void*)&thr,
+                          (void*)&hist0, (void*)&sel, (void*)&D2w, (void*)&hist12, (void*)&ebuf,
+                          (void*)&bcnt, (void*)&cix, (void*)&cnt, (void*)&comb, (void*)&X,
+                          (void*)&ksg, (void*)&pri, (void*)&prw, (void*)&qix, (void*)&acc, (void*)&out };
+        hipError_t rc = hipLaunchCooperativeKernel(reinterpret_cast<const void*>(&k_coop),
+                                                   dim3(CGRID), dim3(256), cargs, 0, stream);
+        if (rc == hipSuccess) done = true; else coop_ok = 0;
+    }
+    if (!done) {
+        hipLaunchKernelGGL(fb_thrscan, dim3(257), dim3(256), 0, stream, samp, hist0, sel, thr);
+        hipLaunchKernelGGL(fb_h1,      dim3(256), dim3(256), 0, stream, D2w, sel, hist12);
+        hipLaunchKernelGGL(fb_h2,      dim3(256), dim3(256), 0, stream, D2w, hist12, sel);
+        hipLaunchKernelGGL(fb_mmdfilt, dim3(512), dim3(256), 0, stream, tqsw, xbf, xn, thr, ebuf, bcnt, D2w, hist12, sel, acc);
+        hipLaunchKernelGGL(fb_scat,    dim3(128), dim3(256), 0, stream, ebuf, bcnt, cix, cnt);
+        hipLaunchKernelGGL(fb_resc,    dim3(CGRID), dim3(256), 0, stream, comb, X, xn, cix, cnt, ksg);
+        hipLaunchKernelGGL(fb_post,    dim3(256), dim3(256), 0, stream, comb, X, cix, cnt, ksg, pri, prw, qix, acc);
+        hipLaunchKernelGGL(fb_final,   dim3(1),   dim3(64),  0, stream, acc, out);
+    }
+}
```
